# Kernel tuning notes

Measured on AMD Instinct MI355X. Metric: run time of the kernel, lower is better.

The kernel has to match this reference:

```python
import jax, jax.numpy as jnp
import numpy as np

N_NODES = 100000
N_EDGES = 1600000
IN_CH, HID_CH, OUT_CH = 512, 128, 128


def gcn_conv(x, src, dst, deg_isqrt, W, b, n_nodes):
    # PyG GCNConv: linear transform, then symmetric-normalized scatter-add
    h = x @ W  # [N, F_out]
    norm = deg_isqrt[src] * deg_isqrt[dst]  # [E+N]
    msg = h[src] * norm[:, None]  # gather + scale
    out = jax.ops.segment_sum(msg, dst, num_segments=n_nodes)
    return out + b


def setup_inputs() -> dict:
    key = jax.random.key(0)
    k1, k2, k3, k4 = jax.random.split(key, 4)
    x = jax.random.normal(k1, (N_NODES, IN_CH), dtype=jnp.float32)
    edge_index = jax.random.randint(k2, (2, N_EDGES), 0, N_NODES, dtype=jnp.int64)
    # Glorot-ish init for weights
    W1 = jax.random.normal(k3, (IN_CH, HID_CH), dtype=jnp.float32) / np.sqrt(IN_CH)
    W2 = jax.random.normal(k4, (HID_CH, OUT_CH), dtype=jnp.float32) / np.sqrt(HID_CH)
    b1 = jnp.zeros((HID_CH,), dtype=jnp.float32)
    b2 = jnp.zeros((OUT_CH,), dtype=jnp.float32)
    return {"x": x, "edge_index": edge_index, "W1": W1, "b1": b1, "W2": W2, "b2": b2}


def reference(x, edge_index, W1, b1, W2, b2):
    n_nodes = x.shape[0]
    # add self-loops (PyG default add_self_loops=True)
    loops = jnp.arange(n_nodes, dtype=edge_index.dtype)
    src = jnp.concatenate([edge_index[0], loops])
    dst = jnp.concatenate([edge_index[1], loops])
    # degree (in-degree over edges incl. self-loops), shared by both layers
    deg = jax.ops.segment_sum(jnp.ones_like(dst, dtype=x.dtype), dst, num_segments=n_nodes)
    deg_isqrt = jax.lax.rsqrt(deg)  # deg >= 1 thanks to self-loops
    h = gcn_conv(x, src, dst, deg_isqrt, W1, b1, n_nodes)
    h = jax.nn.relu(h)
    out = gcn_conv(h, src, dst, deg_isqrt, W2, b2, n_nodes)
    return out
```

## Files before the change

### kernel.cpp

```cpp
#include <hip/hip_runtime.h>
#include <hip/hip_bf16.h>

#define CH 128
#define IN_CH_K 512
#define CHUNK 2048
#define BPAD 5120

typedef short s16x8 __attribute__((ext_vector_type(8)));
typedef float f32x4 __attribute__((ext_vector_type(4)));

__device__ __forceinline__ unsigned int f2bf(float f) {
    unsigned int u = __builtin_bit_cast(unsigned int, f);
    return (u + 0x7fffu + ((u >> 16) & 1u)) >> 16;
}
__device__ __forceinline__ unsigned int pk2bf(float lo, float hi) {
    unsigned int r;
    asm("v_cvt_pk_bf16_f32 %0, %1, %2" : "=v"(r) : "v"(lo), "v"(hi));
    return r;
}
__device__ __forceinline__ float bf_lo(unsigned int u) {
    return __builtin_bit_cast(float, u << 16);
}
__device__ __forceinline__ float bf_hi(unsigned int u) {
    return __builtin_bit_cast(float, u & 0xFFFF0000u);
}
__device__ __forceinline__ unsigned int relu_pk(unsigned int w) {
    unsigned int keep = (~w) & 0x80008000u;
    unsigned int mask = keep - (keep >> 15);
    return w & mask;
}

__global__ void init_cursor_kernel(int* __restrict__ cursor, int NB) {
    int i = blockIdx.x * blockDim.x + threadIdx.x;
    if (i < NB) cursor[i] = i * BPAD;
}

__global__ void bin_kernel(const int* __restrict__ src, const int* __restrict__ dst,
                           int* __restrict__ cursor, int* __restrict__ binned,
                           int E, int NB) {
    __shared__ int h[512];
    __shared__ int base[512];
    __shared__ int cur[512];
    const int tid = threadIdx.x;
    for (int i = tid; i < NB; i += 256) h[i] = 0;
    __syncthreads();

    const int E4 = E >> 2;
    const int beg4 = blockIdx.x * (CHUNK / 4);
    const int end4 = min(E4, beg4 + CHUNK / 4);
    const int4* dst4 = reinterpret_cast<const int4*>(dst);
    const int4* src4 = reinterpret_cast<const int4*>(src);
    const bool last = (blockIdx.x == gridDim.x - 1);

    for (int e4 = beg4 + tid; e4 < end4; e4 += 256) {
        int4 d = dst4[e4];
        atomicAdd(&h[d.x >> 8], 1);
        atomicAdd(&h[d.y >> 8], 1);
        atomicAdd(&h[d.z >> 8], 1);
        atomicAdd(&h[d.w >> 8], 1);
    }
    if (last) {
        for (int e = (E & ~3) + tid; e < E; e += 256)
            atomicAdd(&h[dst[e] >> 8], 1);
    }
    __syncthreads();
    for (int i = tid; i < NB; i += 256) {
        cur[i] = 0;
        if (h[i]) base[i] = atomicAdd(&cursor[i], h[i]);
    }
    __syncthreads();

    for (int e4 = beg4 + tid; e4 < end4; e4 += 256) {
        int4 d = dst4[e4];
        int4 s = src4[e4];
        int b, r, idx;
        b = d.x >> 8; r = atomicAdd(&cur[b], 1); idx = base[b] + r;
        if (idx < (b + 1) * BPAD) binned[idx] = s.x | ((d.x & 255) << 17);
        b = d.y >> 8; r = atomicAdd(&cur[b], 1); idx = base[b] + r;
        if (idx < (b + 1) * BPAD) binned[idx] = s.y | ((d.y & 255) << 17);
        b = d.z >> 8; r = atomicAdd(&cur[b], 1); idx = base[b] + r;
        if (idx < (b + 1) * BPAD) binned[idx] = s.z | ((d.z & 255) << 17);
        b = d.w >> 8; r = atomicAdd(&cur[b], 1); idx = base[b] + r;
        if (idx < (b + 1) * BPAD) binned[idx] = s.w | ((d.w & 255) << 17);
    }
    if (last) {
        for (int e = (E & ~3) + tid; e < E; e += 256) {
            int d = dst[e];
            int b = d >> 8;
            int r = atomicAdd(&cur[b], 1);
            int idx = base[b] + r;
            if (idx < (b + 1) * BPAD) binned[idx] = src[e] | ((d & 255) << 17);
        }
    }
}

__global__ void csr_bucket_kernel(const int* __restrict__ binned, const int* __restrict__ cursor,
                                  int2* __restrict__ row_range, int* __restrict__ csr_src,
                                  float* __restrict__ dinv, int N) {
    __shared__ int cnt[256];
    __shared__ int off[256];
    __shared__ int cur[256];
    const int k = blockIdx.x;
    const int t = threadIdx.x;
    cnt[t] = 0;
    __syncthreads();
    const int beg = k * BPAD;
    const int end = min(cursor[k], (k + 1) * BPAD);
    const int nv = (end - beg) & ~3;
    const int4* b4 = reinterpret_cast<const int4*>(binned + beg);

    for (int q = t; q * 4 < nv; q += 256) {
        int4 p = b4[q];
        atomicAdd(&cnt[p.x >> 17], 1);
        atomicAdd(&cnt[p.y >> 17], 1);
        atomicAdd(&cnt[p.z >> 17], 1);
        atomicAdd(&cnt[p.w >> 17], 1);
    }
    for (int e = beg + nv + t; e < end; e += 256)
        atomicAdd(&cnt[binned[e] >> 17], 1);
    __syncthreads();
    int v = cnt[t];
    off[t] = v;
    __syncthreads();
    #pragma unroll
    for (int o = 1; o < 256; o <<= 1) {
        int tv = (t >= o) ? off[t - o] : 0;
        __syncthreads();
        off[t] += tv;
        __syncthreads();
    }
    int ex = off[t] - v;
    int node = k * 256 + t;
    if (node < N) {
        row_range[node] = make_int2(beg + ex, beg + ex + v);
        dinv[node] = rsqrtf((float)(v + 1));
    }
    cur[t] = ex;
    __syncthreads();
    for (int q = t; q * 4 < nv; q += 256) {
        int4 p = b4[q];
        int dl, r;
        dl = p.x >> 17; r = atomicAdd(&cur[dl], 1); csr_src[beg + r] = p.x & 0x1FFFF;
        dl = p.y >> 17; r = atomicAdd(&cur[dl], 1); csr_src[beg + r] = p.y & 0x1FFFF;
        dl = p.z >> 17; r = atomicAdd(&cur[dl], 1); csr_src[beg + r] = p.z & 0x1FFFF;
        dl = p.w >> 17; r = atomicAdd(&cur[dl], 1); csr_src[beg + r] = p.w & 0x1FFFF;
    }
    for (int e = beg + nv + t; e < end; e += 256) {
        int p = binned[e];
        int dl = p >> 17;
        int r = atomicAdd(&cur[dl], 1);
        csr_src[beg + r] = p & 0x1FFFF;
    }
}

template<bool PERM>
__global__ void convert_w_kernel(const float* __restrict__ W, uint4* __restrict__ WT, int K) {
    int i = blockIdx.x * blockDim.x + threadIdx.x;
    int ng = K >> 3;
    if (i >= ng * CH) return;
    int g = i >> 7;
    int col = i & 127;
    unsigned int h[8];
    #pragma unroll
    for (int j = 0; j < 8; ++j) {
        int kp = g * 8 + j;
        int k = PERM ? ((kp >> 3) + ((kp & 7) << 4)) : kp;
        h[j] = f2bf(W[(size_t)k * CH + col]);
    }
    uint4 v;
    v.x = h[0] | (h[1] << 16);
    v.y = h[2] | (h[3] << 16);
    v.z = h[4] | (h[5] << 16);
    v.w = h[6] | (h[7] << 16);
    WT[i] = v;
}

__launch_bounds__(256, 4)
__global__ void gemm1_mfma_kernel(const float* __restrict__ A, const uint4* __restrict__ WT,
                                  const float* __restrict__ dinv, unsigned short* __restrict__ C,
                                  int M) {
    const int tid = threadIdx.x;
    const int wid = tid >> 6;
    const int lane = tid & 63;
    const int l15 = lane & 15;
    const int lg = lane >> 4;

    const int wave_row = blockIdx.x * 64 + wid * 16;
    const int arow = min(wave_row + l15, M - 1);
    const float4* ap = reinterpret_cast<const float4*>(A + (size_t)arow * IN_CH_K) + lg * 2;
    const uint4* wp = WT + (size_t)lg * CH + l15;

    f32x4 acc[8];
    #pragma unroll
    for (int n = 0; n < 8; ++n) acc[n] = (f32x4){0.f, 0.f, 0.f, 0.f};

    float4 a0 = ap[0], a1 = ap[1];

    #pragma unroll
    for (int ks = 0; ks < 16; ++ks) {
        float4 na0, na1;
        if (ks < 15) {
            na0 = ap[(ks + 1) * 8];
            na1 = ap[(ks + 1) * 8 + 1];
        }

        const uint4* wpk = wp + (size_t)ks * 4 * CH;
        uint4 bw[8];
        #pragma unroll
        for (int n = 0; n < 8; ++n) bw[n] = wpk[n * 16];

        uint4 pk;
        pk.x = pk2bf(a0.x, a0.y);
        pk.y = pk2bf(a0.z, a0.w);
        pk.z = pk2bf(a1.x, a1.y);
        pk.w = pk2bf(a1.z, a1.w);
        s16x8 af = __builtin_bit_cast(s16x8, pk);

        #pragma unroll
        for (int n = 0; n < 8; ++n) {
            s16x8 b = __builtin_bit_cast(s16x8, bw[n]);
            acc[n] = __builtin_amdgcn_mfma_f32_16x16x32_bf16(af, b, acc[n], 0, 0, 0);
        }

        if (ks < 15) { a0 = na0; a1 = na1; }
    }

    #pragma unroll
    for (int i = 0; i < 4; ++i) {
        int row = wave_row + lg * 4 + i;
        if (row < M) {
            float s = dinv[row];
            uint4 v;
            v.x = pk2bf(acc[0][i] * s, acc[1][i] * s);
            v.y = pk2bf(acc[2][i] * s, acc[3][i] * s);
            v.z = pk2bf(acc[4][i] * s, acc[5][i] * s);
            v.w = pk2bf(acc[6][i] * s, acc[7][i] * s);
            *reinterpret_cast<uint4*>(&C[(size_t)row * CH + l15 * 8]) = v;
        }
    }
}

__launch_bounds__(256)
__global__ void gemm2_mfma_kernel(const unsigned short* __restrict__ A, const uint4* __restrict__ WT,
                                  const float* __restrict__ dinv, unsigned short* __restrict__ C,
                                  int M) {
    const int tid = threadIdx.x;
    const int wid = tid >> 6;
    const int lane = tid & 63;
    const int l15 = lane & 15;
    const int lg = lane >> 4;

    const int block_row = blockIdx.x * 128 + wid * 32;

    f32x4 acc[2][8];
    #pragma unroll
    for (int m = 0; m < 2; ++m)
        #pragma unroll
        for (int n = 0; n < 8; ++n)
            acc[m][n] = (f32x4){0.f, 0.f, 0.f, 0.f};

    int arow0 = min(block_row + l15, M - 1);
    int arow1 = min(block_row + 16 + l15, M - 1);
    const uint4* ap0 = reinterpret_cast<const uint4*>(A + (size_t)arow0 * CH);
    const uint4* ap1 = reinterpret_cast<const uint4*>(A + (size_t)arow1 * CH);

    #pragma unroll
    for (int k0 = 0; k0 < CH; k0 += 32) {
        const int fi = (k0 >> 3) + lg;
        uint4 r0 = ap0[fi];
        uint4 r1 = ap1[fi];
        r0.x = relu_pk(r0.x); r0.y = relu_pk(r0.y); r0.z = relu_pk(r0.z); r0.w = relu_pk(r0.w);
        r1.x = relu_pk(r1.x); r1.y = relu_pk(r1.y); r1.z = relu_pk(r1.z); r1.w = relu_pk(r1.w);
        s16x8 a0 = __builtin_bit_cast(s16x8, r0);
        s16x8 a1 = __builtin_bit_cast(s16x8, r1);
        #pragma unroll
        for (int n = 0; n < 8; ++n) {
            uint4 bv = WT[(size_t)fi * CH + n * 16 + l15];
            s16x8 b = __builtin_bit_cast(s16x8, bv);
            acc[0][n] = __builtin_amdgcn_mfma_f32_16x16x32_bf16(a0, b, acc[0][n], 0, 0, 0);
            acc[1][n] = __builtin_amdgcn_mfma_f32_16x16x32_bf16(a1, b, acc[1][n], 0, 0, 0);
        }
    }

    #pragma unroll
    for (int m = 0; m < 2; ++m) {
        #pragma unroll
        for (int i = 0; i < 4; ++i) {
            int row = block_row + m * 16 + lg * 4 + i;
            if (row < M) {
                float s = dinv[row];
                uint4 v;
                v.x = pk2bf(acc[m][0][i] * s, acc[m][1][i] * s);
                v.y = pk2bf(acc[m][2][i] * s, acc[m][3][i] * s);
                v.z = pk2bf(acc[m][4][i] * s, acc[m][5][i] * s);
                v.w = pk2bf(acc[m][6][i] * s, acc[m][7][i] * s);
                *reinterpret_cast<uint4*>(&C[(size_t)row * CH + l15 * 8]) = v;
            }
        }
    }
}

#define GATHER(cc) g[(size_t)__builtin_amdgcn_readfirstlane(cc) * 64 + lane]
template<bool OUT_BF16>
__launch_bounds__(256)
__global__ void aggregate_kernel(const unsigned int* __restrict__ g, const int2* __restrict__ row_range,
                                 const int* __restrict__ csr_src, const float* __restrict__ dinv,
                                 const float* __restrict__ bias, void* __restrict__ outp, int N) {
    const int gtid = blockIdx.x * blockDim.x + threadIdx.x;
    const int node = gtid >> 6;
    if (node >= N) return;
    const int lane = threadIdx.x & 63;

    unsigned int su = g[(size_t)node * 64 + lane];
    const int2 rr = row_range[node];
    float ax = bf_lo(su);
    float ay = bf_hi(su);

    int j = rr.x;
    const int end = rr.y;

    if (j + 8 <= end) {
        int c0 = csr_src[j], c1 = csr_src[j+1], c2 = csr_src[j+2], c3 = csr_src[j+3];
        int c4 = csr_src[j+4], c5 = csr_src[j+5], c6 = csr_src[j+6], c7 = csr_src[j+7];
        j += 8;
        while (j + 8 <= end) {
            int n0 = csr_src[j], n1 = csr_src[j+1], n2 = csr_src[j+2], n3 = csr_src[j+3];
            int n4 = csr_src[j+4], n5 = csr_src[j+5], n6 = csr_src[j+6], n7 = csr_src[j+7];
            j += 8;
            unsigned int u0 = GATHER(c0), u1 = GATHER(c1), u2 = GATHER(c2), u3 = GATHER(c3);
            unsigned int u4 = GATHER(c4), u5 = GATHER(c5), u6 = GATHER(c6), u7 = GATHER(c7);
            ax += ((bf_lo(u0) + bf_lo(u1)) + (bf_lo(u2) + bf_lo(u3)))
                + ((bf_lo(u4) + bf_lo(u5)) + (bf_lo(u6) + bf_lo(u7)));
            ay += ((bf_hi(u0) + bf_hi(u1)) + (bf_hi(u2) + bf_hi(u3)))
                + ((bf_hi(u4) + bf_hi(u5)) + (bf_hi(u6) + bf_hi(u7)));
            c0 = n0; c1 = n1; c2 = n2; c3 = n3;
            c4 = n4; c5 = n5; c6 = n6; c7 = n7;
        }
        unsigned int u0 = GATHER(c0), u1 = GATHER(c1), u2 = GATHER(c2), u3 = GATHER(c3);
        unsigned int u4 = GATHER(c4), u5 = GATHER(c5), u6 = GATHER(c6), u7 = GATHER(c7);
        ax += ((bf_lo(u0) + bf_lo(u1)) + (bf_lo(u2) + bf_lo(u3)))
            + ((bf_lo(u4) + bf_lo(u5)) + (bf_lo(u6) + bf_lo(u7)));
        ay += ((bf_hi(u0) + bf_hi(u1)) + (bf_hi(u2) + bf_hi(u3)))
            + ((bf_hi(u4) + bf_hi(u5)) + (bf_hi(u6) + bf_hi(u7)));
    }
    for (; j + 2 <= end; j += 2) {
        int c0 = csr_src[j], c1 = csr_src[j+1];
        unsigned int u0 = GATHER(c0), u1 = GATHER(c1);
        ax += bf_lo(u0) + bf_lo(u1);
        ay += bf_hi(u0) + bf_hi(u1);
    }
    if (j < end) {
        int c0 = csr_src[j];
        unsigned int u0 = GATHER(c0);
        ax += bf_lo(u0);
        ay += bf_hi(u0);
    }

    const int cp0 = lane << 1;
    const int cp1 = cp0 | 1;
    const int c0 = (cp0 >> 3) + ((cp0 & 7) << 4);
    const int c1 = (cp1 >> 3) + ((cp1 & 7) << 4);
    const float di = dinv[node];
    float ox = di * ax + bias[c0];
    float oy = di * ay + bias[c1];
    if (OUT_BF16) {
        ((unsigned int*)outp)[(size_t)node * 64 + lane] = pk2bf(ox, oy);
    } else {
        float* o = (float*)outp + (size_t)node * CH;
        o[c0] = ox;
        o[c1] = oy;
    }
}

extern "C" void kernel_launch(void* const* d_in, const int* in_sizes, int n_in,
                              void* d_out, int out_size, void* d_ws, size_t ws_size,
                              hipStream_t stream) {
    const float* x  = (const float*)d_in[0];
    const int*   ei = (const int*)d_in[1];
    const float* W1 = (const float*)d_in[2];
    const float* b1 = (const float*)d_in[3];
    const float* W2 = (const float*)d_in[4];
    const float* b2 = (const float*)d_in[5];
    float* out = (float*)d_out;

    const int N = in_sizes[0] / IN_CH_K;
    const int E = in_sizes[1] / 2;
    const int* e_src = ei;
    const int* e_dst = ei + E;

    const int NB = (N + 255) >> 8;
    const int NCHUNK = (E + CHUNK - 1) / CHUNK;

    char* w = (char*)d_ws;
    auto alloc = [&](size_t bytes) {
        char* p = w;
        w += (bytes + 255) & ~(size_t)255;
        return p;
    };
    int*   cursor    = (int*)  alloc((size_t)NB * 4);
    int2*  row_range = (int2*) alloc((size_t)N * 8);
    float* dinv      = (float*)alloc((size_t)N * 4);
    int*   csr_src   = (int*)  alloc((size_t)NB * BPAD * 4);
    uint4* w1t       = (uint4*)alloc((size_t)(IN_CH_K / 8) * CH * 16);
    uint4* w2t       = (uint4*)alloc((size_t)(CH / 8) * CH * 16);
    unsigned short* gbuf = (unsigned short*)alloc((size_t)N * CH * 2);
    unsigned short* abuf = (unsigned short*)alloc((size_t)N * CH * 2);
    int* binned = (int*)gbuf;

    init_cursor_kernel<<<(NB + 255) / 256, 256, 0, stream>>>(cursor, NB);
    bin_kernel<<<NCHUNK, 256, 0, stream>>>(e_src, e_dst, cursor, binned, E, NB);
    csr_bucket_kernel<<<NB, 256, 0, stream>>>(binned, cursor, row_range, csr_src, dinv, N);
    convert_w_kernel<false><<<(IN_CH_K / 8 * CH + 255) / 256, 256, 0, stream>>>(W1, w1t, IN_CH_K);
    convert_w_kernel<true><<<(CH / 8 * CH + 255) / 256, 256, 0, stream>>>(W2, w2t, CH);

    const int gemm1_grid = (N + 63) / 64;
    const int gemm2_grid = (N + 127) / 128;
    const int agg_grid = (N * 64 + 255) / 256;

    gemm1_mfma_kernel<<<gemm1_grid, 256, 0, stream>>>(x, w1t, dinv, gbuf, N);
    aggregate_kernel<true><<<agg_grid, 256, 0, stream>>>((const unsigned int*)gbuf, row_range,
                                                         csr_src, dinv, b1, abuf, N);

    gemm2_mfma_kernel<<<gemm2_grid, 256, 0, stream>>>(abuf, w2t, dinv, gbuf, N);
    aggregate_kernel<false><<<agg_grid, 256, 0, stream>>>((const unsigned int*)gbuf, row_range,
                                                          csr_src, dinv, b2, out, N);
}
```

Baseline: 286.8 us.

## Stage GEMM1 A tiles into LDS via direct global-to-LDS loads

GEMM1 now copies each block's 32x512 fp32 A tile into padded LDS using global_load_lds, then every wave computes two 16-column groups for all 32 rows, reading A from LDS. Before, each wave streamed its own A rows from global memory and loaded all 8 B column tiles per k-step. The aim is more coalesced, asynchronous A loads and less B traffic per wave. In exchange it uses 66KB of LDS per block with occupancy bound 2, more blocks, and narrower 4-byte output stores.

```diff
diff --git a/kernel.cpp b/kernel.cpp
--- a/kernel.cpp
+++ b/kernel.cpp
@@ -175,67 +175,79 @@
     WT[i] = v;
 }
 
-__launch_bounds__(256, 4)
+#define G1B 1040
+__launch_bounds__(256, 2)
 __global__ void gemm1_mfma_kernel(const float* __restrict__ A, const uint4* __restrict__ WT,
                                   const float* __restrict__ dinv, unsigned short* __restrict__ C,
                                   int M) {
+    __shared__ unsigned char lds_raw[64 * G1B];
+
     const int tid = threadIdx.x;
     const int wid = tid >> 6;
     const int lane = tid & 63;
+    const int block_row = blockIdx.x * 32;
+
+    {
+        int grow = block_row + (lane >> 1);
+        if (grow >= M) grow = M - 1;
+        const float* gbase = A + (size_t)grow * IN_CH_K + (lane & 1) * 4;
+        #pragma unroll
+        for (int i = 0; i < 16; ++i) {
+            const int g = wid * 16 + i;
+            const float* gp = gbase + g * 8;
+            void* lp = (void*)&lds_raw[g * G1B];
+            __builtin_amdgcn_global_load_lds(
+                (const __attribute__((address_space(1))) void*)gp,
+                (__attribute__((address_space(3))) void*)lp, 16, 0, 0);
+        }
+    }
+    __syncthreads();
+
     const int l15 = lane & 15;
     const int lg = lane >> 4;
-
-    const int wave_row = blockIdx.x * 64 + wid * 16;
-    const int arow = min(wave_row + l15, M - 1);
-    const float4* ap = reinterpret_cast<const float4*>(A + (size_t)arow * IN_CH_K) + lg * 2;
-    const uint4* wp = WT + (size_t)lg * CH + l15;
-
-    f32x4 acc[8];
-    #pragma unroll
-    for (int n = 0; n < 8; ++n) acc[n] = (f32x4){0.f, 0.f, 0.f, 0.f};
-
-    float4 a0 = ap[0], a1 = ap[1];
-
-    #pragma unroll
+    const int ncol = wid * 2;
+
+    f32x4 acc[2][2];
+    #pragma unroll
+    for (int m = 0; m < 2; ++m)
+        #pragma unroll
+        for (int n = 0; n < 2; ++n)
+            acc[m][n] = (f32x4){0.f, 0.f, 0.f, 0.f};
+
+    #pragma unroll 4
     for (int ks = 0; ks < 16; ++ks) {
-        float4 na0, na1;
-        if (ks < 15) {
-            na0 = ap[(ks + 1) * 8];
-            na1 = ap[(ks + 1) * 8 + 1];
-        }
-
-        const uint4* wpk = wp + (size_t)ks * 4 * CH;
-        uint4 bw[8];
-        #pragma unroll
-        for (int n = 0; n < 8; ++n) bw[n] = wpk[n * 16];
-
-        uint4 pk;
-        pk.x = pk2bf(a0.x, a0.y);
-        pk.y = pk2bf(a0.z, a0.w);
-        pk.z = pk2bf(a1.x, a1.y);
-        pk.w = pk2bf(a1.z, a1.w);
-        s16x8 af = __builtin_bit_cast(s16x8, pk);
-
-        #pragma unroll
-        for (int n = 0; n < 8; ++n) {
-            s16x8 b = __builtin_bit_cast(s16x8, bw[n]);
-            acc[n] = __builtin_amdgcn_mfma_f32_16x16x32_bf16(af, b, acc[n], 0, 0, 0);
-        }
-
-        if (ks < 15) { a0 = na0; a1 = na1; }
-    }
-
-    #pragma unroll
-    for (int i = 0; i < 4; ++i) {
-        int row = wave_row + lg * 4 + i;
-        if (row < M) {
-            float s = dinv[row];
-            uint4 v;
-            v.x = pk2bf(acc[0][i] * s, acc[1][i] * s);
-            v.y = pk2bf(acc[2][i] * s, acc[3][i] * s);
-            v.z = pk2bf(acc[4][i] * s, acc[5][i] * s);
-            v.w = pk2bf(acc[6][i] * s, acc[7][i] * s);
-            *reinterpret_cast<uint4*>(&C[(size_t)row * CH + l15 * 8]) = v;
+        const int g = ks * 4 + lg;
+        uint4 b0v = WT[(size_t)g * CH + ncol * 16 + l15];
+        uint4 b1v = WT[(size_t)g * CH + (ncol + 1) * 16 + l15];
+        s16x8 b0 = __builtin_bit_cast(s16x8, b0v);
+        s16x8 b1 = __builtin_bit_cast(s16x8, b1v);
+
+        #pragma unroll
+        for (int m = 0; m < 2; ++m) {
+            const unsigned abase = (unsigned)(g * G1B + (m * 16 + l15) * 32);
+            f32x4 fa0 = *reinterpret_cast<const f32x4*>(&lds_raw[abase]);
+            f32x4 fa1 = *reinterpret_cast<const f32x4*>(&lds_raw[abase + 16]);
+            uint4 pk;
+            pk.x = pk2bf(fa0[0], fa0[1]);
+            pk.y = pk2bf(fa0[2], fa0[3]);
+            pk.z = pk2bf(fa1[0], fa1[1]);
+            pk.w = pk2bf(fa1[2], fa1[3]);
+            s16x8 af = __builtin_bit_cast(s16x8, pk);
+            acc[m][0] = __builtin_amdgcn_mfma_f32_16x16x32_bf16(af, b0, acc[m][0], 0, 0, 0);
+            acc[m][1] = __builtin_amdgcn_mfma_f32_16x16x32_bf16(af, b1, acc[m][1], 0, 0, 0);
+        }
+    }
+
+    #pragma unroll
+    for (int m = 0; m < 2; ++m) {
+        #pragma unroll
+        for (int i = 0; i < 4; ++i) {
+            int row = block_row + m * 16 + lg * 4 + i;
+            if (row < M) {
+                float s = dinv[row];
+                unsigned pk = pk2bf(acc[m][0][i] * s, acc[m][1][i] * s);
+                *reinterpret_cast<unsigned*>(&C[(size_t)row * CH + l15 * 8 + ncol]) = pk;
+            }
         }
     }
 }
@@ -413,7 +425,7 @@
     convert_w_kernel<false><<<(IN_CH_K / 8 * CH + 255) / 256, 256, 0, stream>>>(W1, w1t, IN_CH_K);
     convert_w_kernel<true><<<(CH / 8 * CH + 255) / 256, 256, 0, stream>>>(W2, w2t, CH);
 
-    const int gemm1_grid = (N + 63) / 64;
+    const int gemm1_grid = (N + 31) / 32;
     const int gemm2_grid = (N + 127) / 128;
     const int agg_grid = (N * 64 + 255) / 256;
 
```

Measured after the change: 276.9 us. 1.04x faster.
